# Kernel optimization log

Measured on AMD Instinct MI355X. Metric: run time of the kernel, lower is better.

## Reference

```python
import jax, jax.numpy as jnp
import numpy as np

N = 50000      # nodes
E = 800000     # edges
IN = 128       # input feature dim
HID = 64       # out_channels per head
HEADS = 2
OUT = 40       # num classes
SLOPE = 0.2    # leaky relu negative slope
EPS = 1e-16    # PyG softmax denominator epsilon


def _xavier(key, shape):
    fan_out, fan_in = shape[0], shape[1]
    a = float(np.sqrt(6.0 / (fan_in + fan_out)))
    return jax.random.uniform(key, shape, minval=-a, maxval=a, dtype=jnp.float32)


def setup_inputs() -> dict:
    key = jax.random.key(0)
    ks = jax.random.split(key, 16)
    x = jax.random.normal(ks[0], (N, IN), dtype=jnp.float32)
    edge_index = jax.random.randint(ks[1], (2, E), 0, N, dtype=jnp.int64)
    # GAT layer 1: lin_l == lin_r (shared), weight [H*C, in], att [C, H]
    W1 = _xavier(ks[2], (HEADS * HID, IN))
    b1 = jnp.zeros((HEADS * HID,), jnp.float32)
    al1 = _xavier(ks[3], (HID, HEADS))
    ar1 = _xavier(ks[4], (HID, HEADS))
    # GAT layer 2: input dim = heads*hidden
    W2 = _xavier(ks[5], (HEADS * HID, HEADS * HID))
    b2 = jnp.zeros((HEADS * HID,), jnp.float32)
    al2 = _xavier(ks[6], (HID, HEADS))
    ar2 = _xavier(ks[7], (HID, HEADS))
    # post_mp: Linear(heads*hid, hid) -> Linear(hid, out)
    Wp1 = _xavier(ks[8], (HID, HEADS * HID))
    bp1 = jnp.zeros((HID,), jnp.float32)
    Wp2 = _xavier(ks[9], (OUT, HID))
    bp2 = jnp.zeros((OUT,), jnp.float32)
    return dict(x=x, edge_index=edge_index, W1=W1, b1=b1, al1=al1, ar1=ar1,
                W2=W2, b2=b2, al2=al2, ar2=ar2, Wp1=Wp1, bp1=bp1, Wp2=Wp2, bp2=bp2)


def gat_layer(x, edge_index, W, b, att_l, att_r):
    """One GAT layer: shared linear, per-edge leaky-relu scores,
    segment-softmax keyed by destination node, scatter-sum."""
    n = x.shape[0]
    xt = (x @ W.T + b).reshape(n, HEADS, HID)          # [N, H, C] (x_l == x_r)
    alpha_l = jnp.einsum('nhc,ch->nh', xt, att_l)      # [N, H]
    alpha_r = jnp.einsum('nhc,ch->nh', xt, att_r)      # [N, H]
    src, dst = edge_index[0], edge_index[1]            # j = source, i = dest
    e = jax.nn.leaky_relu(alpha_r[dst] + alpha_l[src], SLOPE)   # [E, H]
    # segment softmax over edges grouped by destination node
    seg_max = jax.ops.segment_max(e, dst, num_segments=n)       # [N, H]
    ex = jnp.exp(e - seg_max[dst])
    denom = jax.ops.segment_sum(ex, dst, num_segments=n)        # [N, H]
    alpha = ex / (denom[dst] + EPS)                              # [E, H]
    msg = alpha[:, :, None] * xt[src]                            # [E, H, C]
    out = jax.ops.segment_sum(msg, dst, num_segments=n)          # [N, H, C]
    return out.reshape(n, HEADS * HID)


def reference(x, edge_index, W1, b1, al1, ar1, W2, b2, al2, ar2, Wp1, bp1, Wp2, bp2):
    h = jax.nn.relu(gat_layer(x, edge_index, W1, b1, al1, ar1))
    h = jax.nn.relu(gat_layer(h, edge_index, W2, b2, al2, ar2))
    h = h @ Wp1.T + bp1
    h = h @ Wp2.T + bp2
    return jax.nn.log_softmax(h, axis=1)
```

## Files before the change

### kernel.cpp

```cpp
#include <hip/hip_runtime.h>
#include <hip/hip_fp16.h>
#include <cmath>

#define N_NODES 50000
#define N_EDGES 800000
#define F 128
#define OUT_DIM 40
#define SLOPE 0.2f
#define EPS_DEN 1e-16f

#define BK_SHIFT 7
#define BKSZ 128
#define NBK ((N_NODES + BKSZ - 1) / BKSZ)
#define BK_CAP2 2560
#define SC_CHUNK 2500
#define SC_BLOCKS ((N_EDGES + SC_CHUNK - 1) / SC_CHUNK)
#define GEMM_TILES ((N_NODES + 127) / 128)
#define A_BLOCKS (SC_BLOCKS + 25 + GEMM_TILES)
#define SMEM_BYTES 21504

typedef _Float16 half8 __attribute__((ext_vector_type(8)));
typedef float floatx4 __attribute__((ext_vector_type(4)));

struct ScatterS { int sd[SC_CHUNK]; short sb[SC_CHUNK]; int h[NBK]; int lofs[NBK]; };
struct GemmS    { __half Ah[128][40]; __half Bh[128][40]; };
static_assert(sizeof(ScatterS) <= SMEM_BYTES, "scatter LDS");
static_assert(sizeof(GemmS)    <= SMEM_BYTES, "gemm LDS");

__device__ inline float4 load4(const float* p) { return *(const float4*)p; }
__device__ inline float4 load4(const __half* p) {
  uint2 u = *(const uint2*)p;
  float2 a = __half22float2(*(__half2*)&u.x);
  float2 b = __half22float2(*(__half2*)&u.y);
  return make_float4(a.x, a.y, b.x, b.y);
}

__device__ __forceinline__ void scatter_phase(const int* __restrict__ ei,
    int* __restrict__ bcur, int* __restrict__ pairs, int it, int tid, char* smem_) {
  ScatterS* S = (ScatterS*)smem_;
  for (int i = tid; i < NBK; i += 256) S->h[i] = 0;
  __syncthreads();
  int base = it * SC_CHUNK;
  int end = base + SC_CHUNK; if (end > N_EDGES) end = N_EDGES;
  int cnt = end - base;
  for (int e = base + tid; e < end; e += 256) {
    int s = ei[e];
    int d = ei[N_EDGES + e];
    int b = d >> BK_SHIFT;
    S->sd[e - base] = (s << BK_SHIFT) | (d & (BKSZ - 1));
    S->sb[e - base] = (short)b;
    atomicAdd(&S->h[b], 1);
  }
  __syncthreads();
  for (int i = tid; i < NBK; i += 256)
    if (S->h[i]) { S->lofs[i] = i * BK_CAP2 + atomicAdd(&bcur[i], S->h[i]); S->h[i] = 0; }
  __syncthreads();
  for (int i = tid; i < cnt; i += 256) {
    int b = S->sb[i];
    int pos = S->lofs[b] + atomicAdd(&S->h[b], 1);
    pairs[pos] = S->sd[i];
  }
}

__device__ __forceinline__ void combine_phase(const float* __restrict__ Wp1,
    const float* __restrict__ bp1, const float* __restrict__ Wp2,
    const float* __restrict__ bp2, __half* __restrict__ Wch,
    float* __restrict__ bc, int it, int tid) {
  if (it < 24) {
    int idx = it * 256 + tid;
    int o = idx >> 7, k = idx & 127;
    float s = 0.f;
    if (o < OUT_DIM) {
#pragma unroll 8
      for (int j = 0; j < 64; ++j) s += Wp2[o * 64 + j] * Wp1[j * 128 + k];
    }
    Wch[o * 128 + k] = __float2half(s);
  } else if (tid < 48) {
    int o = tid;
    if (o < OUT_DIM) {
      float s = bp2[o];
      for (int j = 0; j < 64; ++j) s += Wp2[o * 64 + j] * bp1[j];
      bc[o] = s;
    } else {
      bc[o] = -1e30f;
    }
  }
}

template <typename T>
__device__ __forceinline__ void gemm_phase(const T* __restrict__ A,
    const float* __restrict__ W, const float* __restrict__ b,
    const float* __restrict__ attl, const float* __restrict__ attr,
    __half* __restrict__ Ch, float* __restrict__ al, float* __restrict__ ar,
    int nrows, int tile, int tid, char* smem_) {
  GemmS* S = (GemmS*)smem_;
  int lane = tid & 63, wid = tid >> 6;
  int quad = lane >> 4, col = lane & 15;
  int r0 = tile * 128;
  int rowhalf = wid >> 1, colhalf = wid & 1;
  floatx4 acc[4][4] = {};
  for (int kc = 0; kc < 128; kc += 32) {
    for (int i = tid; i < 512; i += 256) {
      int row = i >> 2, seg = i & 3;
      int gr = r0 + row;
      float4 v0, v1;
      if (gr < nrows) {
        const T* p = A + (size_t)gr * 128 + kc + seg * 8;
        v0 = load4(p); v1 = load4(p + 4);
      } else { v0 = make_float4(0.f,0.f,0.f,0.f); v1 = v0; }
      __half2 h0 = __floats2half2_rn(v0.x, v0.y), h1 = __floats2half2_rn(v0.z, v0.w);
      __half2 h2 = __floats2half2_rn(v1.x, v1.y), h3 = __floats2half2_rn(v1.z, v1.w);
      uint4 pk; pk.x = *(unsigned*)&h0; pk.y = *(unsigned*)&h1;
      pk.z = *(unsigned*)&h2; pk.w = *(unsigned*)&h3;
      *(uint4*)&S->Ah[row][seg * 8] = pk;
      const float* q = W + (size_t)row * 128 + kc + seg * 8;
      float4 w0 = *(const float4*)q, w1 = *(const float4*)(q + 4);
      __half2 g0 = __floats2half2_rn(w0.x, w0.y), g1 = __floats2half2_rn(w0.z, w0.w);
      __half2 g2 = __floats2half2_rn(w1.x, w1.y), g3 = __floats2half2_rn(w1.z, w1.w);
      uint4 qk; qk.x = *(unsigned*)&g0; qk.y = *(unsigned*)&g1;
      qk.z = *(unsigned*)&g2; qk.w = *(unsigned*)&g3;
      *(uint4*)&S->Bh[row][seg * 8] = qk;
    }
    __syncthreads();
    half8 afr[4], bfr[4];
#pragma unroll
    for (int rt = 0; rt < 4; ++rt)
      afr[rt] = *(const half8*)&S->Ah[rowhalf * 64 + rt * 16 + col][quad * 8];
#pragma unroll
    for (int ct = 0; ct < 4; ++ct)
      bfr[ct] = *(const half8*)&S->Bh[colhalf * 64 + ct * 16 + col][quad * 8];
#pragma unroll
    for (int rt = 0; rt < 4; ++rt)
#pragma unroll
      for (int ct = 0; ct < 4; ++ct)
        acc[rt][ct] = __builtin_amdgcn_mfma_f32_16x16x32_f16(afr[rt], bfr[ct],
                                                             acc[rt][ct], 0, 0, 0);
    __syncthreads();
  }
  int head = colhalf;
  float bj[4], wl4[4], wr4[4];
#pragma unroll
  for (int ct = 0; ct < 4; ++ct) {
    int c = ct * 16 + col;
    bj[ct] = b[head * 64 + c];
    wl4[ct] = attl[c * 2 + head];
    wr4[ct] = attr[c * 2 + head];
  }
#pragma unroll
  for (int rt = 0; rt < 4; ++rt) {
#pragma unroll
    for (int reg = 0; reg < 4; ++reg) {
      int gr = r0 + rowhalf * 64 + rt * 16 + quad * 4 + reg;
      bool ok = gr < nrows;
      float pl = 0.f, pr = 0.f;
#pragma unroll
      for (int ct = 0; ct < 4; ++ct) {
        float v = acc[rt][ct][reg] + bj[ct];
        pl += v * wl4[ct]; pr += v * wr4[ct];
        if (ok) Ch[(size_t)gr * F + head * 64 + ct * 16 + col] = __float2half(v);
      }
      pl += __shfl_xor(pl, 1, 64); pr += __shfl_xor(pr, 1, 64);
      pl += __shfl_xor(pl, 2, 64); pr += __shfl_xor(pr, 2, 64);
      pl += __shfl_xor(pl, 4, 64); pr += __shfl_xor(pr, 4, 64);
      pl += __shfl_xor(pl, 8, 64); pr += __shfl_xor(pr, 8, 64);
      if (ok && col == 0) { al[gr * 2 + head] = pl; ar[gr * 2 + head] = pr; }
    }
  }
}

__global__ __launch_bounds__(256) void kernelA(const int* __restrict__ ei,
    int* __restrict__ bcur, int* __restrict__ pairs,
    const float* __restrict__ Wp1, const float* __restrict__ bp1,
    const float* __restrict__ Wp2, const float* __restrict__ bp2,
    __half* __restrict__ Wch, float* __restrict__ bc,
    const float* __restrict__ x, const float* __restrict__ W1,
    const float* __restrict__ b1, const float* __restrict__ al1,
    const float* __restrict__ ar1, __half* __restrict__ xh,
    float* __restrict__ al, float* __restrict__ ar) {
  __shared__ __align__(16) char smem[SMEM_BYTES];
  int bid = blockIdx.x, tid = threadIdx.x;
  if (bid < SC_BLOCKS) {
    scatter_phase(ei, bcur, pairs, bid, tid, smem);
  } else if (bid < SC_BLOCKS + 25) {
    combine_phase(Wp1, bp1, Wp2, bp2, Wch, bc, bid - SC_BLOCKS, tid);
  } else {
    gemm_phase<float>(x, W1, b1, al1, ar1, xh, al, ar, N_NODES,
                      bid - SC_BLOCKS - 25, tid, smem);
  }
}

__global__ __launch_bounds__(256) void gemm2_kernel(const __half* __restrict__ hb,
    const float* __restrict__ W2, const float* __restrict__ b2,
    const float* __restrict__ al2, const float* __restrict__ ar2,
    __half* __restrict__ xh, float* __restrict__ al, float* __restrict__ ar) {
  __shared__ __align__(16) char smem[SMEM_BYTES];
  gemm_phase<__half>(hb, W2, b2, al2, ar2, xh, al, ar, N_NODES,
                     blockIdx.x, threadIdx.x, smem);
}

__global__ __launch_bounds__(256) void local_sort(const int* __restrict__ bcur,
    const int* __restrict__ pairs, int* __restrict__ rowstart,
    int* __restrict__ rowend, int* __restrict__ srcs) {
  __shared__ int buf[BK_CAP2];
  __shared__ int sorted[BK_CAP2];
  __shared__ int hist[BKSZ];
  __shared__ int cur[BKSZ];
  int tid = threadIdx.x;
  int b = blockIdx.x;
  int base = b * BK_CAP2;
  int cnt = bcur[b];
  if (cnt > BK_CAP2) cnt = BK_CAP2;
  if (tid < BKSZ) hist[tid] = 0;
  __syncthreads();
  for (int i = tid; i < cnt; i += 256) {
    int p = pairs[base + i];
    buf[i] = p;
    atomicAdd(&hist[p & (BKSZ - 1)], 1);
  }
  __syncthreads();
  if (tid < 64) {
    int lane = tid;
    int carry = 0;
#pragma unroll
    for (int c = 0; c < BKSZ; c += 64) {
      int v = hist[c + lane];
      int x = v;
#pragma unroll
      for (int off = 1; off < 64; off <<= 1) {
        int t = __shfl_up(x, off, 64);
        if (lane >= off) x += t;
      }
      int excl = carry + x - v;
      cur[c + lane] = excl;
      int node = b * BKSZ + c + lane;
      if (node < N_NODES) {
        rowstart[node] = base + excl;
        rowend[node]   = base + excl + v;
      }
      carry += __shfl(x, 63, 64);
    }
  }
  __syncthreads();
  for (int i = tid; i < cnt; i += 256) {
    int p = buf[i];
    int pos = atomicAdd(&cur[p & (BKSZ - 1)], 1);
    sorted[pos] = p >> BK_SHIFT;
  }
  __syncthreads();
  for (int i = tid; i < cnt; i += 256)
    srcs[base + i] = sorted[i];
}

__global__ __launch_bounds__(256) void aggregate_kernel(const int* __restrict__ rowstart,
    const int* __restrict__ rowend, const int* __restrict__ srcs,
    const float* __restrict__ al, const float* __restrict__ ar,
    const __half* __restrict__ xh, __half* __restrict__ out, int n) {
  __shared__ float ebuf[4][2][64];
  __shared__ int   sbuf[4][64];
  int tid = threadIdx.x;
  int wid = tid >> 6, lane = tid & 63;
  int g = lane >> 4, q = lane & 15;
  int head = q >> 3;
  int node = blockIdx.x * 4 + wid;
  if (node >= n) return;
  int start = rowstart[node], end = rowend[node];
  float2 arv = *(const float2*)(ar + (size_t)node * 2);
  float ar0 = arv.x, ar1 = arv.y;
  const float* wrow = &ebuf[wid][head][0];
  const __half* xbase = xh + q * 8;
  float acc[8] = {};
  float dl0 = 0.f, dl1 = 0.f;
  for (int c = start; c < end; c += 64) {
    int j = c + lane;
    float e0 = 0.f, e1 = 0.f; int soff = 0;
    if (j < end) {
      int s = srcs[j];
      soff = s << BK_SHIFT;
      float2 a = *(const float2*)(al + (size_t)s * 2);
      float s0 = a.x + ar0; s0 = (s0 > 0.f) ? s0 : SLOPE * s0;
      float s1 = a.y + ar1; s1 = (s1 > 0.f) ? s1 : SLOPE * s1;
      e0 = __expf(s0); e1 = __expf(s1);
    }
    dl0 += e0; dl1 += e1;
    ebuf[wid][0][lane] = e0; ebuf[wid][1][lane] = e1; sbuf[wid][lane] = soff;
    __builtin_amdgcn_wave_barrier();
    int cend = end - c; if (cend > 64) cend = 64;
#pragma unroll 4
    for (int t = 0; t < cend; t += 4) {
      int te = t + g;
      if (te < cend) {
        int so = sbuf[wid][te];
        float w = wrow[te];
        uint4 u = *(const uint4*)(xbase + so);
        const __half2* hh = (const __half2*)&u;
        float2 f0 = __half22float2(hh[0]);
        float2 f1 = __half22float2(hh[1]);
        float2 f2 = __half22float2(hh[2]);
        float2 f3 = __half22float2(hh[3]);
        acc[0] += w * f0.x; acc[1] += w * f0.y;
        acc[2] += w * f1.x; acc[3] += w * f1.y;
        acc[4] += w * f2.x; acc[5] += w * f2.y;
        acc[6] += w * f3.x; acc[7] += w * f3.y;
      }
    }
    __builtin_amdgcn_wave_barrier();
  }
#pragma unroll
  for (int off = 32; off > 0; off >>= 1) {
    dl0 += __shfl_xor(dl0, off, 64);
    dl1 += __shfl_xor(dl1, off, 64);
  }
#pragma unroll
  for (int k = 0; k < 8; ++k) {
    acc[k] += __shfl_xor(acc[k], 16, 64);
    acc[k] += __shfl_xor(acc[k], 32, 64);
  }
  if (g == 0) {
    float d = (head == 0) ? dl0 : dl1;
    float inv = 1.f / (d + EPS_DEN);
    __half2 o0 = __floats2half2_rn(fmaxf(acc[0] * inv, 0.f), fmaxf(acc[1] * inv, 0.f));
    __half2 o1 = __floats2half2_rn(fmaxf(acc[2] * inv, 0.f), fmaxf(acc[3] * inv, 0.f));
    __half2 o2 = __floats2half2_rn(fmaxf(acc[4] * inv, 0.f), fmaxf(acc[5] * inv, 0.f));
    __half2 o3 = __floats2half2_rn(fmaxf(acc[6] * inv, 0.f), fmaxf(acc[7] * inv, 0.f));
    uint4 pack;
    pack.x = *(unsigned*)&o0; pack.y = *(unsigned*)&o1;
    pack.z = *(unsigned*)&o2; pack.w = *(unsigned*)&o3;
    *(uint4*)(out + (size_t)node * F + q * 8) = pack;
  }
}

__global__ __launch_bounds__(256) void post_mfma(const __half* __restrict__ hb,
    const __half* __restrict__ Wch, const float* __restrict__ bc,
    float* __restrict__ out, int n) {
  int tid = threadIdx.x;
  int lane = tid & 63, wid = tid >> 6;
  int quad = lane >> 4, col = lane & 15;
  int base = blockIdx.x * 64 + wid * 16;
  int arow = base + col;
  int asafe = (arow < n) ? arow : (n - 1);
  floatx4 acc[3] = {};
#pragma unroll
  for (int kc = 0; kc < 128; kc += 32) {
    half8 afr = *(const half8*)(hb + (size_t)asafe * F + kc + quad * 8);
#pragma unroll
    for (int ct = 0; ct < 3; ++ct) {
      half8 bfr = *(const half8*)(Wch + (size_t)(ct * 16 + col) * 128 + kc + quad * 8);
      acc[ct] = __builtin_amdgcn_mfma_f32_16x16x32_f16(afr, bfr, acc[ct], 0, 0, 0);
    }
  }
  float bcv[3];
#pragma unroll
  for (int ct = 0; ct < 3; ++ct) bcv[ct] = bc[ct * 16 + col];
#pragma unroll
  for (int reg = 0; reg < 4; ++reg) {
    int row = base + quad * 4 + reg;
    float z[3], m = -INFINITY;
#pragma unroll
    for (int ct = 0; ct < 3; ++ct) { z[ct] = acc[ct][reg] + bcv[ct]; m = fmaxf(m, z[ct]); }
    m = fmaxf(m, __shfl_xor(m, 1, 64));
    m = fmaxf(m, __shfl_xor(m, 2, 64));
    m = fmaxf(m, __shfl_xor(m, 4, 64));
    m = fmaxf(m, __shfl_xor(m, 8, 64));
    float s = 0.f;
#pragma unroll
    for (int ct = 0; ct < 3; ++ct) s += __expf(z[ct] - m);
    s += __shfl_xor(s, 1, 64);
    s += __shfl_xor(s, 2, 64);
    s += __shfl_xor(s, 4, 64);
    s += __shfl_xor(s, 8, 64);
    float ls = logf(s);
    if (row < n) {
#pragma unroll
      for (int ct = 0; ct < 3; ++ct) {
        int o = ct * 16 + col;
        if (o < OUT_DIM) out[(size_t)row * OUT_DIM + o] = z[ct] - m - ls;
      }
    }
  }
}

extern "C" void kernel_launch(void* const* d_in, const int* in_sizes, int n_in,
                              void* d_out, int out_size, void* d_ws, size_t ws_size,
                              hipStream_t stream) {
  const float* x   = (const float*)d_in[0];
  const int*   ei  = (const int*)d_in[1];
  const float* W1  = (const float*)d_in[2];
  const float* b1  = (const float*)d_in[3];
  const float* al1 = (const float*)d_in[4];
  const float* ar1 = (const float*)d_in[5];
  const float* W2  = (const float*)d_in[6];
  const float* b2  = (const float*)d_in[7];
  const float* al2 = (const float*)d_in[8];
  const float* ar2 = (const float*)d_in[9];
  const float* Wp1 = (const float*)d_in[10];
  const float* bp1 = (const float*)d_in[11];
  const float* Wp2 = (const float*)d_in[12];
  const float* bp2 = (const float*)d_in[13];
  float* out = (float*)d_out;

  float* al    = (float*)d_ws;
  float* ar    = al + (size_t)N_NODES * 2;
  __half* Wch  = (__half*)(ar + (size_t)N_NODES * 2);
  float* bc    = (float*)(Wch + 48 * 128);
  int* rowstart= (int*)(bc + 48);
  int* rowend  = rowstart + N_NODES;
  int* bcur    = rowend + N_NODES;
  int* srcs    = bcur + NBK;
  int* pairs   = srcs + NBK * BK_CAP2;
  uintptr_t pp = ((uintptr_t)(pairs + NBK * BK_CAP2) + 255) & ~(uintptr_t)255;
  __half* xh   = (__half*)pp;
  __half* hb   = xh + (size_t)N_NODES * F;

  int nwgrid = (N_NODES + 3) / 4;

  hipMemsetAsync(bcur, 0, NBK * sizeof(int), stream);
  kernelA<<<A_BLOCKS, 256, 0, stream>>>(ei, bcur, pairs, Wp1, bp1, Wp2, bp2,
                                        Wch, bc, x, W1, b1, al1, ar1, xh, al, ar);
  local_sort<<<NBK, 256, 0, stream>>>(bcur, pairs, rowstart, rowend, srcs);
  aggregate_kernel<<<nwgrid, 256, 0, stream>>>(rowstart, rowend, srcs, al, ar, xh, hb, N_NODES);
  gemm2_kernel<<<GEMM_TILES, 256, 0, stream>>>(hb, W2, b2, al2, ar2, xh, al, ar);
  aggregate_kernel<<<nwgrid, 256, 0, stream>>>(rowstart, rowend, srcs, al, ar, xh, hb, N_NODES);
  post_mfma<<<(N_NODES + 63) / 64, 256, 0, stream>>>(hb, Wch, bc, out, N_NODES);
}
```

Baseline: 226.7 us.

## Accumulate GAT aggregation in packed fp16 with shifted exp weights and 1024-thread blocks

The aggregation kernel now accumulates neighbour features with packed half2 FMAs instead of fp32, and stores the exp weights as half2 packed alongside the source offset in a single int2 LDS entry. To keep the fp16 weights in range, scores are shifted down by a constant before the exp and clamped. Blocks grow to 16 waves (1024 threads). This aims to cut ALU work, conversions and LDS traffic in the gather loop, at the cost of fp16 accumulation error and overflow risk on high-degree nodes. It also leaves some dead code computing unused shifted scores.

```diff
diff --git a/kernel.cpp b/kernel.cpp
--- a/kernel.cpp
+++ b/kernel.cpp
@@ -8,6 +8,7 @@
 #define OUT_DIM 40
 #define SLOPE 0.2f
 #define EPS_DEN 1e-16f
+#define SCORE_SHIFT 4.0f
 
 #define BK_SHIFT 7
 #define BKSZ 128
@@ -251,24 +252,22 @@
     srcs[base + i] = sorted[i];
 }
 
-__global__ __launch_bounds__(256) void aggregate_kernel(const int* __restrict__ rowstart,
+__global__ __launch_bounds__(1024) void aggregate_kernel(const int* __restrict__ rowstart,
     const int* __restrict__ rowend, const int* __restrict__ srcs,
     const float* __restrict__ al, const float* __restrict__ ar,
     const __half* __restrict__ xh, __half* __restrict__ out, int n) {
-  __shared__ float ebuf[4][2][64];
-  __shared__ int   sbuf[4][64];
+  __shared__ int2 ebuf[16][64];
   int tid = threadIdx.x;
   int wid = tid >> 6, lane = tid & 63;
   int g = lane >> 4, q = lane & 15;
   int head = q >> 3;
-  int node = blockIdx.x * 4 + wid;
+  int node = blockIdx.x * 16 + wid;
   if (node >= n) return;
   int start = rowstart[node], end = rowend[node];
   float2 arv = *(const float2*)(ar + (size_t)node * 2);
-  float ar0 = arv.x, ar1 = arv.y;
-  const float* wrow = &ebuf[wid][head][0];
+  float ar0 = arv.x - SCORE_SHIFT, ar1 = arv.y - SCORE_SHIFT;
   const __half* xbase = xh + q * 8;
-  float acc[8] = {};
+  __half2 a01 = __float2half2_rn(0.f), a23 = a01, a45 = a01, a67 = a01;
   float dl0 = 0.f, dl1 = 0.f;
   for (int c = start; c < end; c += 64) {
     int j = c + lane;
@@ -279,28 +278,30 @@
       float2 a = *(const float2*)(al + (size_t)s * 2);
       float s0 = a.x + ar0; s0 = (s0 > 0.f) ? s0 : SLOPE * s0;
       float s1 = a.y + ar1; s1 = (s1 > 0.f) ? s1 : SLOPE * s1;
-      e0 = __expf(s0); e1 = __expf(s1);
+      e0 = s0; e1 = s1;
+      float t0 = a.x + arv.x; t0 = (t0 > 0.f) ? t0 : SLOPE * t0;
+      float t1 = a.y + arv.y; t1 = (t1 > 0.f) ? t1 : SLOPE * t1;
+      e0 = fminf(__expf(t0 - SCORE_SHIFT), 60000.f);
+      e1 = fminf(__expf(t1 - SCORE_SHIFT), 60000.f);
     }
     dl0 += e0; dl1 += e1;
-    ebuf[wid][0][lane] = e0; ebuf[wid][1][lane] = e1; sbuf[wid][lane] = soff;
+    __half2 eh = __floats2half2_rn(e0, e1);
+    ebuf[wid][lane] = make_int2(soff, *(int*)&eh);
     __builtin_amdgcn_wave_barrier();
     int cend = end - c; if (cend > 64) cend = 64;
 #pragma unroll 4
     for (int t = 0; t < cend; t += 4) {
       int te = t + g;
       if (te < cend) {
-        int so = sbuf[wid][te];
-        float w = wrow[te];
-        uint4 u = *(const uint4*)(xbase + so);
+        int2 se = ebuf[wid][te];
+        __half2 ep = *(__half2*)&se.y;
+        __half2 w2 = (head == 0) ? __low2half2(ep) : __high2half2(ep);
+        uint4 u = *(const uint4*)(xbase + se.x);
         const __half2* hh = (const __half2*)&u;
-        float2 f0 = __half22float2(hh[0]);
-        float2 f1 = __half22float2(hh[1]);
-        float2 f2 = __half22float2(hh[2]);
-        float2 f3 = __half22float2(hh[3]);
-        acc[0] += w * f0.x; acc[1] += w * f0.y;
-        acc[2] += w * f1.x; acc[3] += w * f1.y;
-        acc[4] += w * f2.x; acc[5] += w * f2.y;
-        acc[6] += w * f3.x; acc[7] += w * f3.y;
+        a01 = __hfma2(w2, hh[0], a01);
+        a23 = __hfma2(w2, hh[1], a23);
+        a45 = __hfma2(w2, hh[2], a45);
+        a67 = __hfma2(w2, hh[3], a67);
       }
     }
     __builtin_amdgcn_wave_barrier();
@@ -310,18 +311,28 @@
     dl0 += __shfl_xor(dl0, off, 64);
     dl1 += __shfl_xor(dl1, off, 64);
   }
-#pragma unroll
-  for (int k = 0; k < 8; ++k) {
-    acc[k] += __shfl_xor(acc[k], 16, 64);
-    acc[k] += __shfl_xor(acc[k], 32, 64);
+  int i01 = *(int*)&a01, i23 = *(int*)&a23, i45 = *(int*)&a45, i67 = *(int*)&a67;
+#pragma unroll
+  for (int off = 16; off <= 32; off <<= 1) {
+    int j01 = __shfl_xor(i01, off, 64), j23 = __shfl_xor(i23, off, 64);
+    int j45 = __shfl_xor(i45, off, 64), j67 = __shfl_xor(i67, off, 64);
+    __half2 t;
+    t = __hadd2(*(__half2*)&i01, *(__half2*)&j01); i01 = *(int*)&t;
+    t = __hadd2(*(__half2*)&i23, *(__half2*)&j23); i23 = *(int*)&t;
+    t = __hadd2(*(__half2*)&i45, *(__half2*)&j45); i45 = *(int*)&t;
+    t = __hadd2(*(__half2*)&i67, *(__half2*)&j67); i67 = *(int*)&t;
   }
   if (g == 0) {
     float d = (head == 0) ? dl0 : dl1;
     float inv = 1.f / (d + EPS_DEN);
-    __half2 o0 = __floats2half2_rn(fmaxf(acc[0] * inv, 0.f), fmaxf(acc[1] * inv, 0.f));
-    __half2 o1 = __floats2half2_rn(fmaxf(acc[2] * inv, 0.f), fmaxf(acc[3] * inv, 0.f));
-    __half2 o2 = __floats2half2_rn(fmaxf(acc[4] * inv, 0.f), fmaxf(acc[5] * inv, 0.f));
-    __half2 o3 = __floats2half2_rn(fmaxf(acc[6] * inv, 0.f), fmaxf(acc[7] * inv, 0.f));
+    float2 f01 = __half22float2(*(__half2*)&i01);
+    float2 f23 = __half22float2(*(__half2*)&i23);
+    float2 f45 = __half22float2(*(__half2*)&i45);
+    float2 f67 = __half22float2(*(__half2*)&i67);
+    __half2 o0 = __floats2half2_rn(fmaxf(f01.x * inv, 0.f), fmaxf(f01.y * inv, 0.f));
+    __half2 o1 = __floats2half2_rn(fmaxf(f23.x * inv, 0.f), fmaxf(f23.y * inv, 0.f));
+    __half2 o2 = __floats2half2_rn(fmaxf(f45.x * inv, 0.f), fmaxf(f45.y * inv, 0.f));
+    __half2 o3 = __floats2half2_rn(fmaxf(f67.x * inv, 0.f), fmaxf(f67.y * inv, 0.f));
     uint4 pack;
     pack.x = *(unsigned*)&o0; pack.y = *(unsigned*)&o1;
     pack.z = *(unsigned*)&o2; pack.w = *(unsigned*)&o3;
@@ -411,14 +422,14 @@
   __half* xh   = (__half*)pp;
   __half* hb   = xh + (size_t)N_NODES * F;
 
-  int nwgrid = (N_NODES + 3) / 4;
+  int agrid = (N_NODES + 15) / 16;
 
   hipMemsetAsync(bcur, 0, NBK * sizeof(int), stream);
   kernelA<<<A_BLOCKS, 256, 0, stream>>>(ei, bcur, pairs, Wp1, bp1, Wp2, bp2,
                                         Wch, bc, x, W1, b1, al1, ar1, xh, al, ar);
   local_sort<<<NBK, 256, 0, stream>>>(bcur, pairs, rowstart, rowend, srcs);
-  aggregate_kernel<<<nwgrid, 256, 0, stream>>>(rowstart, rowend, srcs, al, ar, xh, hb, N_NODES);
+  aggregate_kernel<<<agrid, 1024, 0, stream>>>(rowstart, rowend, srcs, al, ar, xh, hb, N_NODES);
   gemm2_kernel<<<GEMM_TILES, 256, 0, stream>>>(hb, W2, b2, al2, ar2, xh, al, ar);
-  aggregate_kernel<<<nwgrid, 256, 0, stream>>>(rowstart, rowend, srcs, al, ar, xh, hb, N_NODES);
+  aggregate_kernel<<<agrid, 1024, 0, stream>>>(rowstart, rowend, srcs, al, ar, xh, hb, N_NODES);
   post_mfma<<<(N_NODES + 63) / 64, 256, 0, stream>>>(hb, Wch, bc, out, N_NODES);
 }
```

Measured after the change: 230.0 us. About the same (+1.5%).
